# Optimization experiments

Hardware: AMD Instinct MI355X
Metric: run time of the kernel (lower is better)

Reference implementation:

```python
import jax, jax.numpy as jnp
import numpy as np

N = 50000   # function nodes
E = 100000  # edges per relation
H = 8       # heads
D = 96      # per-head dim (768 // 8)
L = 2       # conv layers
B = 256     # graphs in batch
C = 31      # num_classes + 1


def setup_inputs() -> dict:
    key = jax.random.key(0)
    ks = jax.random.split(key, 24)
    s = 0.05  # weight init scale to keep attention logits sane
    inp = {
        "function_feats": jax.random.normal(ks[0], (N, 768), jnp.float32),
        "w_src_calls": jax.random.normal(ks[1], (L, 768, 768), jnp.float32) * s,
        "b_src_calls": jnp.zeros((L, 768), jnp.float32),
        "w_dst_calls": jax.random.normal(ks[2], (L, 768, 768), jnp.float32) * s,
        "b_dst_calls": jnp.zeros((L, 768), jnp.float32),
        "attn_calls": jax.random.normal(ks[3], (L, H, D), jnp.float32) * s,
        "w_src_cb": jax.random.normal(ks[4], (L, 768, 768), jnp.float32) * s,
        "b_src_cb": jnp.zeros((L, 768), jnp.float32),
        "w_dst_cb": jax.random.normal(ks[5], (L, 768, 768), jnp.float32) * s,
        "b_dst_cb": jnp.zeros((L, 768), jnp.float32),
        "attn_cb": jax.random.normal(ks[6], (L, H, D), jnp.float32) * s,
        "fc1_w": jax.random.normal(ks[7], (768, 256), jnp.float32) * s,
        "fc1_b": jnp.zeros((256,), jnp.float32),
        "fc2_w": jax.random.normal(ks[8], (256, C), jnp.float32) * s,
        "fc2_b": jnp.zeros((C,), jnp.float32),
        "calls_src": jax.random.randint(ks[9], (E,), 0, N),
        "calls_dst": jax.random.randint(ks[10], (E,), 0, N),
        "cb_src": jax.random.randint(ks[11], (E,), 0, N),
        "cb_dst": jax.random.randint(ks[12], (E,), 0, N),
        "graph_start_idx": jnp.sort(jax.random.randint(ks[13], (B,), 0, N)),
        "labels": jax.random.randint(ks[14], (B,), 0, C),
    }
    return inp


def _gatv2(h, Ws, bs, Wd, bd, attn, src, dst):
    # DGL GATv2Conv: e_ij = attn . leaky_relu(W_src h_i + W_dst h_j); softmax over in-edges of j
    fs = (h @ Ws + bs).reshape(N, H, D)
    fd = (h @ Wd + bd).reshape(N, H, D)
    e = jax.nn.leaky_relu(fs[src] + fd[dst], negative_slope=0.2)  # [E,H,D]
    score = jnp.einsum('ehd,hd->eh', e, attn)                      # [E,H]
    mx = jax.ops.segment_max(score, dst, num_segments=N)           # [N,H]
    ex = jnp.exp(score - mx[dst])
    den = jax.ops.segment_sum(ex, dst, num_segments=N)
    alpha = ex / den[dst]                                          # edge softmax
    return jax.ops.segment_sum(fs[src] * alpha[..., None], dst, num_segments=N)  # [N,H,D]


def reference(function_feats, w_src_calls, b_src_calls, w_dst_calls, b_dst_calls,
              attn_calls, w_src_cb, b_src_cb, w_dst_cb, b_dst_cb, attn_cb,
              fc1_w, fc1_b, fc2_w, fc2_b,
              calls_src, calls_dst, cb_src, cb_dst, graph_start_idx, labels):
    h = function_feats
    for l in range(L):
        o = _gatv2(h, w_src_calls[l], b_src_calls[l], w_dst_calls[l], b_dst_calls[l],
                   attn_calls[l], calls_src, calls_dst)
        o = o + _gatv2(h, w_src_cb[l], b_src_cb[l], w_dst_cb[l], b_dst_cb[l],
                       attn_cb[l], cb_src, cb_dst)  # HeteroGraphConv 'sum' aggregate
        h = o.reshape(N, H * D) + h                  # residual
    func_embed = h[graph_start_idx]                  # [B,768] gather first node per graph
    logits = jax.nn.relu(func_embed @ fc1_w + fc1_b) @ fc2_w + fc2_b  # [B,C]
    logp = jax.nn.log_softmax(logits, axis=-1)
    loss = -jnp.mean(jnp.take_along_axis(logp, labels[:, None], axis=1))
    return (loss, logits)
```

## Files before the change

kernel.cpp:

```cpp
#include <hip/hip_runtime.h>
#include <hip/hip_bf16.h>
#include <math.h>

#define N_NODES 50000
#define NE      100000
#define FDIM    768
#define NFUSE   3072
#define NB      256
#define NC      31

#define A1_CAP  16384
#define N1_CAP  4096
#define NBLK    ((N_NODES + 255) / 256)
#define EB      ((NE + 255) / 256)
#define GTN     12

#define TWT_BLOCKS  (8 * 576)
#define BIAS_BLOCKS 24
#define CVT_BLOCKS  512
#define SETUP_BLOCKS (TWT_BLOCKS + BIAS_BLOCKS + CVT_BLOCKS)

typedef __hip_bfloat16 bf16;
typedef __attribute__((ext_vector_type(8))) short bf16x8;
typedef __attribute__((ext_vector_type(4))) float f32x4;

__device__ inline float u2f(unsigned short u) { return __uint_as_float(((unsigned int)u) << 16); }
__device__ inline unsigned short f2u(float f) { return __bfloat16_as_ushort(__float2bfloat16(f)); }

__device__ inline void load_lds16(const void* g, void* l) {
    __builtin_amdgcn_global_load_lds(
        (const __attribute__((address_space(1))) void*)g,
        (__attribute__((address_space(3))) void*)l, 16, 0, 0);
}

__global__ __launch_bounds__(256) void mark_gsi_kernel(const int* __restrict__ gsi,
                                                       int* __restrict__ fL2,
                                                       int* __restrict__ fL1,
                                                       int* __restrict__ fA1) {
    const int n = gsi[threadIdx.x];
    fL2[n] = 1; fL1[n] = 1; fA1[n] = 1;
}

__global__ __launch_bounds__(256) void mark2_kernel(const int* __restrict__ src0,
                                                    const int* __restrict__ dst0,
                                                    const int* __restrict__ src1,
                                                    const int* __restrict__ dst1,
                                                    const int* __restrict__ dflag,
                                                    int* __restrict__ f1,
                                                    int* __restrict__ f2) {
    const int e = blockIdx.x * 256 + threadIdx.x;
    if (e >= NE) return;
    const int* src = blockIdx.y ? src1 : src0;
    const int* dst = blockIdx.y ? dst1 : dst0;
    if (dflag[dst[e]]) {
        const int s = src[e];
        f1[s] = 1;
        if (f2) f2[s] = 1;
    }
}

__global__ __launch_bounds__(256) void comphist_kernel(const int* __restrict__ fA1,
                                                       const int* __restrict__ fL1,
                                                       const int* __restrict__ fL2,
                                                       int* __restrict__ list1, int* __restrict__ idx1,
                                                       int* __restrict__ list2, int* __restrict__ idx2,
                                                       int* __restrict__ list0,
                                                       int* __restrict__ cnts,
                                                       const int* __restrict__ dst0,
                                                       const int* __restrict__ dst1,
                                                       int* __restrict__ deg) {
    const int b = blockIdx.x, t = threadIdx.x;
    if (b < NBLK) {
        const int n = b * 256 + t;
        if (n >= N_NODES) return;
        if (fA1[n]) {
            const int p = atomicAdd(&cnts[0], 1);
            if (p < A1_CAP) { list1[p] = n; idx1[n] = p; } else idx1[n] = 0;
        }
        if (fL1[n]) {
            const int p = atomicAdd(&cnts[1], 1);
            if (p < N1_CAP) { list2[p] = n; idx2[n] = p; } else idx2[n] = 0;
        }
        if (fL2[n]) {
            const int p = atomicAdd(&cnts[2], 1);
            if (p < 256) list0[p] = n;
        }
    } else {
        const int eb_id = b - NBLK;
        const int r = (eb_id >= EB) ? 1 : 0;
        const int e = (eb_id - r * EB) * 256 + t;
        if (e < NE) atomicAdd(&deg[(size_t)r * N_NODES + (r ? dst1 : dst0)[e]], 1);
    }
}

__global__ __launch_bounds__(256) void setup_kernel(const float* __restrict__ w_sc,
                                                    const float* __restrict__ w_dc,
                                                    const float* __restrict__ w_scb,
                                                    const float* __restrict__ w_dcb,
                                                    const float* __restrict__ b_sc,
                                                    const float* __restrict__ b_dc,
                                                    const float* __restrict__ b_scb,
                                                    const float* __restrict__ b_dcb,
                                                    const float* __restrict__ feats,
                                                    const int* __restrict__ list,
                                                    const int* __restrict__ pcnt,
                                                    bf16* __restrict__ WtFl,
                                                    float* __restrict__ pb,
                                                    bf16* __restrict__ h) {
    __shared__ float tile[32][33];
    const int b = blockIdx.x;
    const int t = threadIdx.x;
    if (b < TWT_BLOCKS) {
        const int z = b / 576, cell = b % 576;
        const int l = z >> 2, sel2 = z & 3;
        const float* src;
        if (sel2 == 0) src = w_sc; else if (sel2 == 1) src = w_scb;
        else if (sel2 == 2) src = w_dc; else src = w_dcb;
        src += (size_t)l * FDIM * FDIM;
        bf16* dst = WtFl + (size_t)z * FDIM * FDIM;
        const int tx = t & 31, ty = t >> 5;
        const int x0 = (cell % 24) * 32, y0 = (cell / 24) * 32;
#pragma unroll
        for (int q = 0; q < 4; ++q)
            tile[ty + q * 8][tx] = src[(size_t)(y0 + ty + q * 8) * FDIM + x0 + tx];
        __syncthreads();
#pragma unroll
        for (int q = 0; q < 4; ++q)
            dst[(size_t)(x0 + ty + q * 8) * FDIM + y0 + tx] = __float2bfloat16(tile[tx][ty + q * 8]);
    } else if (b < TWT_BLOCKS + BIAS_BLOCKS) {
        const int idx = (b - TWT_BLOCKS) * 256 + t;
        const int l = idx / NFUSE, c = idx % NFUSE;
        const int sel2 = c / FDIM, off = c % FDIM;
        const float* src;
        if (sel2 == 0) src = b_sc; else if (sel2 == 1) src = b_scb;
        else if (sel2 == 2) src = b_dc; else src = b_dcb;
        pb[idx] = src[l * FDIM + off];
    } else {
        int c = *pcnt; if (c > A1_CAP) c = A1_CAP;
        for (int i = b - TWT_BLOCKS - BIAS_BLOCKS; i < c; i += CVT_BLOCKS) {
            const int n = list[i];
            const float* s = feats + (size_t)n * FDIM;
            bf16* d = h + (size_t)n * FDIM;
            for (int k = t; k < FDIM; k += 256) d[k] = __float2bfloat16(s[k]);
        }
    }
}

__global__ __launch_bounds__(256) void gemm2(const bf16* __restrict__ A,
                                             const bf16* __restrict__ Wt,
                                             const float* __restrict__ pb,
                                             bf16* __restrict__ C,
                                             const int* __restrict__ rlA,
                                             const int* __restrict__ cntAp, int capA,
                                             const int* __restrict__ rlB,
                                             const int* __restrict__ cntBp, int capB,
                                             const int* __restrict__ idxmap,
                                             int blocksA) {
    int bid = blockIdx.x;
    const int* rowlist;
    int cnt, col0;
    if (bid < blocksA) {
        rowlist = rlA; cnt = *cntAp; if (cnt > capA) cnt = capA; col0 = 0;
    } else {
        bid -= blocksA;
        rowlist = rlB; cnt = *cntBp; if (cnt > capB) cnt = capB; col0 = 1536;
    }
    const int tm = bid / GTN, tn = bid % GTN;
    const int m0 = tm * 128, n0 = tn * 128;
    if (m0 >= cnt) return;

    __shared__ __align__(16) short Abuf[128 * 64];
    __shared__ __align__(16) short Bbuf[128 * 64];
    const int t = threadIdx.x;
    const int wid = t >> 6, lane = t & 63;
    const int wr = wid >> 1, wc = wid & 1;
    const int lr = lane & 15, lk = lane >> 4;

    const f32x4 zero4 = {0.f, 0.f, 0.f, 0.f};
    f32x4 acc[4][4];
#pragma unroll
    for (int i = 0; i < 4; ++i)
#pragma unroll
        for (int j = 0; j < 4; ++j) acc[i][j] = zero4;

    int arow[4], brow[4], acol[4], ldsoff[4];
#pragma unroll
    for (int i = 0; i < 4; ++i) {
        const int s = i * 256 + t;
        const int rr = s >> 3, pch = s & 7;
        int ri = m0 + rr; if (ri >= cnt) ri = cnt - 1;
        arow[i] = rowlist[ri];
        brow[i] = col0 + n0 + rr;
        acol[i] = (pch ^ (rr & 7)) << 3;
        ldsoff[i] = (i * 256 + wid * 64) * 16;
    }

    for (int kt = 0; kt < FDIM / 64; ++kt) {
        const int k0 = kt * 64;
#pragma unroll
        for (int i = 0; i < 4; ++i) {
            load_lds16(A + (size_t)arow[i] * FDIM + k0 + acol[i], (char*)Abuf + ldsoff[i]);
            load_lds16(Wt + (size_t)brow[i] * FDIM + k0 + acol[i], (char*)Bbuf + ldsoff[i]);
        }
        __syncthreads();
#pragma unroll
        for (int kh = 0; kh < 2; ++kh) {
            bf16x8 av[4], bv[4];
            const int c = kh * 4 + lk;
#pragma unroll
            for (int i = 0; i < 4; ++i) {
                const int mm = wr * 64 + i * 16 + lr;
                av[i] = *(const bf16x8*)((const char*)Abuf + mm * 128 + ((c ^ (mm & 7)) << 4));
            }
#pragma unroll
            for (int j = 0; j < 4; ++j) {
                const int nn = wc * 64 + j * 16 + lr;
                bv[j] = *(const bf16x8*)((const char*)Bbuf + nn * 128 + ((c ^ (nn & 7)) << 4));
            }
#pragma unroll
            for (int i = 0; i < 4; ++i)
#pragma unroll
                for (int j = 0; j < 4; ++j)
                    acc[i][j] = __builtin_amdgcn_mfma_f32_16x16x32_bf16(bv[j], av[i], acc[i][j], 0, 0, 0);
        }
        __syncthreads();
    }

#pragma unroll
    for (int i = 0; i < 4; ++i) {
        const int row = m0 + wr * 64 + i * 16 + lr;
        if (row < cnt) {
            const int crow = idxmap[rowlist[row]];
#pragma unroll
            for (int j = 0; j < 4; ++j) {
                const int col = col0 + n0 + wc * 64 + j * 16 + lk * 4;
                const float4 b4 = *(const float4*)(pb + col);
                ushort4 w;
                w.x = f2u(acc[i][j][0] + b4.x);
                w.y = f2u(acc[i][j][1] + b4.y);
                w.z = f2u(acc[i][j][2] + b4.z);
                w.w = f2u(acc[i][j][3] + b4.w);
                *(ushort4*)(C + (size_t)crow * NFUSE + col) = w;
            }
        }
    }
}

__global__ __launch_bounds__(256) void scan1_kernel(const int* __restrict__ deg,
                                                    int* __restrict__ bsum) {
    const int r = blockIdx.y, b = blockIdx.x, t = threadIdx.x;
    const int i = b * 256 + t;
    __shared__ int s[256];
    s[t] = (i < N_NODES) ? deg[(size_t)r * N_NODES + i] : 0;
    __syncthreads();
    for (int o = 128; o > 0; o >>= 1) {
        if (t < o) s[t] += s[t + o];
        __syncthreads();
    }
    if (t == 0) bsum[r * NBLK + b] = s[0];
}

__global__ __launch_bounds__(256) void scan2_kernel(int* __restrict__ bsum,
                                                    int* __restrict__ boff,
                                                    int* __restrict__ rowp0,
                                                    int* __restrict__ rowp1) {
    const int t = threadIdx.x;
    if (t < 2) {
        int run = 0;
        for (int b = 0; b < NBLK; ++b) {
            boff[t * NBLK + b] = run;
            run += bsum[t * NBLK + b];
        }
    }
    if (t == 0) rowp0[N_NODES] = NE;
    if (t == 1) rowp1[N_NODES] = NE;
}

__global__ __launch_bounds__(256) void scan3_kernel(const int* __restrict__ deg,
                                                    const int* __restrict__ boff,
                                                    int* __restrict__ rowp0, int* __restrict__ cursor0,
                                                    int* __restrict__ rowp1, int* __restrict__ cursor1) {
    const int r = blockIdx.y, b = blockIdx.x, t = threadIdx.x;
    const int i = b * 256 + t;
    int* rowp = r ? rowp1 : rowp0;
    int* cursor = r ? cursor1 : cursor0;
    __shared__ int s[256];
    const int v = (i < N_NODES) ? deg[(size_t)r * N_NODES + i] : 0;
    s[t] = v;
    __syncthreads();
    for (int o = 1; o < 256; o <<= 1) {
        int x = 0;
        if (t >= o) x = s[t - o];
        __syncthreads();
        if (t >= o) s[t] += x;
        __syncthreads();
    }
    if (i < N_NODES) {
        const int p = boff[r * NBLK + b] + s[t] - v;
        rowp[i] = p;
        cursor[i] = p;
    }
}

__global__ __launch_bounds__(256) void scatter2_kernel(const int* __restrict__ dst0,
                                                       const int* __restrict__ dst1,
                                                       int* __restrict__ cursor0,
                                                       int* __restrict__ cursor1,
                                                       int* __restrict__ eid0,
                                                       int* __restrict__ eid1) {
    const int e = blockIdx.x * 256 + threadIdx.x;
    const int r = blockIdx.y;
    if (e < NE) {
        if (r == 0) { const int p = atomicAdd(&cursor0[dst0[e]], 1); eid0[p] = e; }
        else        { const int p = atomicAdd(&cursor1[dst1[e]], 1); eid1[p] = e; }
    }
}

__device__ inline void att_accum(const bf16* __restrict__ fsd, const int* __restrict__ idx,
                                 int n, int lane, const float* __restrict__ attn,
                                 const int* __restrict__ rowp, const int* __restrict__ eid,
                                 const int* __restrict__ src, int fs_off, int fd_off,
                                 float* __restrict__ out) {
    float fdv[12], atv[12];
    {
        const ushort4* pfd = (const ushort4*)(fsd + (size_t)idx[n] * NFUSE + fd_off + lane * 12);
        const ushort4 d0 = pfd[0], d1 = pfd[1], d2 = pfd[2];
        fdv[0] = u2f(d0.x); fdv[1] = u2f(d0.y); fdv[2] = u2f(d0.z); fdv[3] = u2f(d0.w);
        fdv[4] = u2f(d1.x); fdv[5] = u2f(d1.y); fdv[6] = u2f(d1.z); fdv[7] = u2f(d1.w);
        fdv[8] = u2f(d2.x); fdv[9] = u2f(d2.y); fdv[10] = u2f(d2.z); fdv[11] = u2f(d2.w);
        const float4* pat = (const float4*)(attn + lane * 12);
        const float4 a0 = pat[0], a1 = pat[1], a2 = pat[2];
        atv[0] = a0.x; atv[1] = a0.y; atv[2] = a0.z; atv[3] = a0.w;
        atv[4] = a1.x; atv[5] = a1.y; atv[6] = a1.z; atv[7] = a1.w;
        atv[8] = a2.x; atv[9] = a2.y; atv[10] = a2.z; atv[11] = a2.w;
    }
    const int beg = rowp[n], end = rowp[n + 1];
    float m = -INFINITY, den = 0.f;
    float acc[12];
#pragma unroll
    for (int j = 0; j < 12; ++j) acc[j] = 0.f;

    for (int i = beg; i < end; ++i) {
        const int e = eid[i];
        const ushort4* pf = (const ushort4*)(fsd + (size_t)idx[src[e]] * NFUSE + fs_off + lane * 12);
        const ushort4 a0 = pf[0], a1 = pf[1], a2 = pf[2];
        float fsv[12];
        fsv[0] = u2f(a0.x); fsv[1] = u2f(a0.y); fsv[2] = u2f(a0.z); fsv[3] = u2f(a0.w);
        fsv[4] = u2f(a1.x); fsv[5] = u2f(a1.y); fsv[6] = u2f(a1.z); fsv[7] = u2f(a1.w);
        fsv[8] = u2f(a2.x); fsv[9] = u2f(a2.y); fsv[10] = u2f(a2.z); fsv[11] = u2f(a2.w);
        float p = 0.f;
#pragma unroll
        for (int j = 0; j < 12; ++j) {
            float x = fsv[j] + fdv[j];
            x = (x > 0.f) ? x : 0.2f * x;
            p += x * atv[j];
        }
        p += __shfl_xor(p, 1);
        p += __shfl_xor(p, 2);
        p += __shfl_xor(p, 4);
        if (p > m) {
            const float sc = expf(m - p);
            den *= sc;
#pragma unroll
            for (int j = 0; j < 12; ++j) acc[j] *= sc;
            m = p;
        }
        const float w = expf(p - m);
        den += w;
#pragma unroll
        for (int j = 0; j < 12; ++j) acc[j] += w * fsv[j];
    }
    const float inv = (den > 0.f) ? 1.f / den : 0.f;
#pragma unroll
    for (int j = 0; j < 12; ++j) out[j] = acc[j] * inv;
}

__global__ __launch_bounds__(256) void aggL_kernel(const bf16* __restrict__ fsd,
                                                   const int* __restrict__ idx,
                                                   const float* __restrict__ attn0,
                                                   const float* __restrict__ attn1,
                                                   const int* __restrict__ rowp0,
                                                   const int* __restrict__ eid0,
                                                   const int* __restrict__ src0,
                                                   const int* __restrict__ rowp1,
                                                   const int* __restrict__ eid1,
                                                   const int* __restrict__ src1,
                                                   bf16* __restrict__ h,
                                                   const int* __restrict__ list,
                                                   const int* __restrict__ pcnt,
                                                   int cap) {
    const int wid = threadIdx.x >> 6;
    const int lane = threadIdx.x & 63;
    int cnt = *pcnt; if (cnt > cap) cnt = cap;
    const int i = blockIdx.x * 4 + wid;
    if (i >= cnt) return;
    const int n = list[i];

    float a0[12], a1[12];
    att_accum(fsd, idx, n, lane, attn0, rowp0, eid0, src0, 0, 1536, a0);
    att_accum(fsd, idx, n, lane, attn1, rowp1, eid1, src1, 768, 2304, a1);

    const size_t base = (size_t)n * FDIM + lane * 12;
    const ushort4* ph = (const ushort4*)(h + base);
    const ushort4 h0 = ph[0], h1 = ph[1], h2 = ph[2];
    ushort4 r0, r1, r2;
    r0.x = f2u(u2f(h0.x) + a0[0] + a1[0]);  r0.y = f2u(u2f(h0.y) + a0[1] + a1[1]);
    r0.z = f2u(u2f(h0.z) + a0[2] + a1[2]);  r0.w = f2u(u2f(h0.w) + a0[3] + a1[3]);
    r1.x = f2u(u2f(h1.x) + a0[4] + a1[4]);  r1.y = f2u(u2f(h1.y) + a0[5] + a1[5]);
    r1.z = f2u(u2f(h1.z) + a0[6] + a1[6]);  r1.w = f2u(u2f(h1.w) + a0[7] + a1[7]);
    r2.x = f2u(u2f(h2.x) + a0[8] + a1[8]);  r2.y = f2u(u2f(h2.y) + a0[9] + a1[9]);
    r2.z = f2u(u2f(h2.z) + a0[10] + a1[10]); r2.w = f2u(u2f(h2.w) + a0[11] + a1[11]);
    ((ushort4*)(h + base))[0] = r0; ((ushort4*)(h + base))[1] = r1; ((ushort4*)(h + base))[2] = r2;
}

__global__ __launch_bounds__(256) void head_kernel(const bf16* __restrict__ h,
                                                   const int* __restrict__ gsi,
                                                   const float* __restrict__ fc1w,
                                                   const float* __restrict__ fc1b,
                                                   const float* __restrict__ fc2w,
                                                   const float* __restrict__ fc2b,
                                                   float* __restrict__ out) {
    __shared__ float fe[FDIM];
    __shared__ float hid[256];
    const int b = blockIdx.x, t = threadIdx.x;
    const int node = gsi[b];
    for (int i = t; i < FDIM; i += 256) fe[i] = __bfloat162float(h[(size_t)node * FDIM + i]);
    __syncthreads();
    float acc = fc1b[t];
    for (int k = 0; k < FDIM; ++k) acc += fe[k] * fc1w[k * 256 + t];
    hid[t] = (acc > 0.f) ? acc : 0.f;
    __syncthreads();
    if (t < NC) {
        float acc2 = fc2b[t];
        for (int k = 0; k < 256; ++k) acc2 += hid[k] * fc2w[k * NC + t];
        out[1 + b * NC + t] = acc2;
    }
}

__global__ __launch_bounds__(256) void loss_kernel(const float* __restrict__ logits,
                                                   const int* __restrict__ labels,
                                                   float* __restrict__ out) {
    __shared__ float red[256];
    const int b = threadIdx.x;
    float m = -INFINITY;
    for (int c = 0; c < NC; ++c) m = fmaxf(m, logits[b * NC + c]);
    float sum = 0.f;
    for (int c = 0; c < NC; ++c) sum += expf(logits[b * NC + c] - m);
    const float lse = m + logf(sum);
    const float ll = logits[b * NC + labels[b]];
    red[b] = lse - ll;
    __syncthreads();
    for (int s = 128; s > 0; s >>= 1) {
        if (b < s) red[b] += red[b + s];
        __syncthreads();
    }
    if (b == 0) out[0] = red[0] / (float)NB;
}

extern "C" void kernel_launch(void* const* d_in, const int* in_sizes, int n_in,
                              void* d_out, int out_size, void* d_ws, size_t ws_size,
                              hipStream_t stream) {
    const float* feats = (const float*)d_in[0];
    const float* fc1w  = (const float*)d_in[11];
    const float* fc1b  = (const float*)d_in[12];
    const float* fc2w  = (const float*)d_in[13];
    const float* fc2b  = (const float*)d_in[14];
    const int* src0    = (const int*)d_in[15];
    const int* dst0    = (const int*)d_in[16];
    const int* src1    = (const int*)d_in[17];
    const int* dst1    = (const int*)d_in[18];
    const int* gsi     = (const int*)d_in[19];
    const int* labels  = (const int*)d_in[20];

    const size_t NF = (size_t)N_NODES * FDIM;
    const size_t WSZ = (size_t)FDIM * FDIM;
    char* p = (char*)d_ws;
    bf16* h    = (bf16*)p;  p += NF * 2;
    bf16* fsd  = (bf16*)p;  p += (size_t)A1_CAP * NFUSE * 2;
    bf16* WtFl = (bf16*)p;  p += 8 * WSZ * 2;
    float* pb  = (float*)p; p += 2 * NFUSE * 4;
    int* flagL2 = (int*)p;  p += (size_t)N_NODES * 4;
    int* flagL1 = (int*)p;  p += (size_t)N_NODES * 4;
    int* flagA1 = (int*)p;  p += (size_t)N_NODES * 4;
    int* cnts   = (int*)p;  p += 64 * 4;
    int* deg    = (int*)p;  p += 2 * (size_t)N_NODES * 4;
    const size_t zero_bytes = (3 * (size_t)N_NODES + 64 + 2 * (size_t)N_NODES) * 4;
    int* idx1  = (int*)p;   p += (size_t)N_NODES * 4;
    int* idx2  = (int*)p;   p += (size_t)N_NODES * 4;
    int* list1 = (int*)p;   p += (size_t)A1_CAP * 4;
    int* list2 = (int*)p;   p += (size_t)N1_CAP * 4;
    int* list0 = (int*)p;   p += 256 * 4;
    int* bsum  = (int*)p;   p += 2 * NBLK * 4;
    int* boff  = (int*)p;   p += 2 * NBLK * 4;
    int* rowp0 = (int*)p;   p += ((size_t)N_NODES + 1) * 4 + 252;
    int* rowp1 = (int*)p;   p += ((size_t)N_NODES + 1) * 4 + 252;
    int* cursor0 = (int*)p; p += (size_t)N_NODES * 4;
    int* cursor1 = (int*)p; p += (size_t)N_NODES * 4;
    int* eid0  = (int*)p;   p += (size_t)NE * 4;
    int* eid1  = (int*)p;   p += (size_t)NE * 4;

    hipMemsetAsync(flagL2, 0, zero_bytes, stream);
    mark_gsi_kernel<<<1, 256, 0, stream>>>(gsi, flagL2, flagL1, flagA1);
    mark2_kernel<<<dim3(EB, 2), 256, 0, stream>>>(src0, dst0, src1, dst1, flagL2, flagL1, flagA1);
    mark2_kernel<<<dim3(EB, 2), 256, 0, stream>>>(src0, dst0, src1, dst1, flagL1, flagA1, (int*)nullptr);
    comphist_kernel<<<NBLK + 2 * EB, 256, 0, stream>>>(
        flagA1, flagL1, flagL2, list1, idx1, list2, idx2, list0, cnts, dst0, dst1, deg);

    scan1_kernel<<<dim3(NBLK, 2), 256, 0, stream>>>(deg, bsum);
    scan2_kernel<<<1, 256, 0, stream>>>(bsum, boff, rowp0, rowp1);
    scan3_kernel<<<dim3(NBLK, 2), 256, 0, stream>>>(deg, boff, rowp0, cursor0, rowp1, cursor1);
    scatter2_kernel<<<dim3(EB, 2), 256, 0, stream>>>(dst0, dst1, cursor0, cursor1, eid0, eid1);

    setup_kernel<<<SETUP_BLOCKS, 256, 0, stream>>>(
        (const float*)d_in[1], (const float*)d_in[3], (const float*)d_in[6], (const float*)d_in[8],
        (const float*)d_in[2], (const float*)d_in[4], (const float*)d_in[7], (const float*)d_in[9],
        feats, list1, &cnts[0], WtFl, pb, h);

    const int blocksA0 = (A1_CAP / 128) * GTN;
    const int blocksB0 = (N1_CAP / 128) * GTN;
    const int blocksA1 = (N1_CAP / 128) * GTN;
    const int blocksB1 = (256 / 128) * GTN;

    gemm2<<<blocksA0 + blocksB0, 256, 0, stream>>>(
        h, WtFl, pb, fsd,
        list1, &cnts[0], A1_CAP, list2, &cnts[1], N1_CAP, idx1, blocksA0);
    aggL_kernel<<<(N1_CAP + 3) / 4, 256, 0, stream>>>(
        fsd, idx1, (const float*)d_in[5], (const float*)d_in[10],
        rowp0, eid0, src0, rowp1, eid1, src1, h, list2, &cnts[1], N1_CAP);

    gemm2<<<blocksA1 + blocksB1, 256, 0, stream>>>(
        h, WtFl + 4 * WSZ, pb + NFUSE, fsd,
        list2, &cnts[1], N1_CAP, list0, &cnts[2], 256, idx2, blocksA1);
    aggL_kernel<<<64, 256, 0, stream>>>(
        fsd, idx2, (const float*)d_in[5] + FDIM, (const float*)d_in[10] + FDIM,
        rowp0, eid0, src0, rowp1, eid1, src1, h, list0, &cnts[2], 256);

    head_kernel<<<NB, 256, 0, stream>>>(h, gsi, fc1w, fc1b, fc2w, fc2b, (float*)d_out);
    loss_kernel<<<1, 256, 0, stream>>>((float*)d_out + 1, labels, (float*)d_out);
}
```

Baseline: 192.4 us.

## Build CSR only for needed destination nodes and fuse final aggregation into head

```diff
diff --git a/kernel.cpp b/kernel.cpp
--- a/kernel.cpp
+++ b/kernel.cpp
@@ -19,6 +19,7 @@
 #define BIAS_BLOCKS 24
 #define CVT_BLOCKS  512
 #define SETUP_BLOCKS (TWT_BLOCKS + BIAS_BLOCKS + CVT_BLOCKS)
+#define SETUPH_BLOCKS (SETUP_BLOCKS + 2 * EB)
 
 typedef __hip_bfloat16 bf16;
 typedef __attribute__((ext_vector_type(8))) short bf16x8;
@@ -33,63 +34,68 @@
         (__attribute__((address_space(3))) void*)l, 16, 0, 0);
 }
 
-__global__ __launch_bounds__(256) void mark_gsi_kernel(const int* __restrict__ gsi,
-                                                       int* __restrict__ fL2,
-                                                       int* __restrict__ fL1,
-                                                       int* __restrict__ fA1) {
-    const int n = gsi[threadIdx.x];
-    fL2[n] = 1; fL1[n] = 1; fA1[n] = 1;
-}
-
-__global__ __launch_bounds__(256) void mark2_kernel(const int* __restrict__ src0,
+__global__ __launch_bounds__(256) void markA_kernel(const int* __restrict__ gsi,
+                                                    const int* __restrict__ src0,
                                                     const int* __restrict__ dst0,
                                                     const int* __restrict__ src1,
                                                     const int* __restrict__ dst1,
-                                                    const int* __restrict__ dflag,
-                                                    int* __restrict__ f1,
-                                                    int* __restrict__ f2) {
+                                                    int* __restrict__ fL1,
+                                                    int* __restrict__ fA1,
+                                                    int* __restrict__ list0,
+                                                    int* __restrict__ cnts) {
+    const int t = threadIdx.x, b = blockIdx.x;
+    if (b == 0) {
+        const int n = gsi[t];
+        fL1[n] = 1; fA1[n] = 1;
+        const bool first = (t == 0) || (gsi[t - 1] != n);
+        if (first) {
+            const int p = atomicAdd(&cnts[2], 1);
+            if (p < 256) list0[p] = n;
+        }
+        return;
+    }
+    __shared__ int g[256];
+    g[t] = gsi[t];
+    __syncthreads();
+    const int eb = b - 1;
+    const int r = (eb >= EB) ? 1 : 0;
+    const int e = (eb - r * EB) * 256 + t;
+    if (e >= NE) return;
+    const int d = (r ? dst1 : dst0)[e];
+    int lo = 0, hi = 256;
+    while (lo < hi) { const int mid = (lo + hi) >> 1; if (g[mid] < d) lo = mid + 1; else hi = mid; }
+    if (lo < 256 && g[lo] == d) {
+        const int s = (r ? src1 : src0)[e];
+        fL1[s] = 1; fA1[s] = 1;
+    }
+}
+
+__global__ __launch_bounds__(256) void markB_kernel(const int* __restrict__ src0,
+                                                    const int* __restrict__ dst0,
+                                                    const int* __restrict__ src1,
+                                                    const int* __restrict__ dst1,
+                                                    const int* __restrict__ fL1,
+                                                    int* __restrict__ fA1) {
     const int e = blockIdx.x * 256 + threadIdx.x;
     if (e >= NE) return;
-    const int* src = blockIdx.y ? src1 : src0;
-    const int* dst = blockIdx.y ? dst1 : dst0;
-    if (dflag[dst[e]]) {
-        const int s = src[e];
-        f1[s] = 1;
-        if (f2) f2[s] = 1;
-    }
-}
-
-__global__ __launch_bounds__(256) void comphist_kernel(const int* __restrict__ fA1,
-                                                       const int* __restrict__ fL1,
-                                                       const int* __restrict__ fL2,
-                                                       int* __restrict__ list1, int* __restrict__ idx1,
-                                                       int* __restrict__ list2, int* __restrict__ idx2,
-                                                       int* __restrict__ list0,
-                                                       int* __restrict__ cnts,
-                                                       const int* __restrict__ dst0,
-                                                       const int* __restrict__ dst1,
-                                                       int* __restrict__ deg) {
-    const int b = blockIdx.x, t = threadIdx.x;
-    if (b < NBLK) {
-        const int n = b * 256 + t;
-        if (n >= N_NODES) return;
-        if (fA1[n]) {
-            const int p = atomicAdd(&cnts[0], 1);
-            if (p < A1_CAP) { list1[p] = n; idx1[n] = p; } else idx1[n] = 0;
-        }
-        if (fL1[n]) {
-            const int p = atomicAdd(&cnts[1], 1);
-            if (p < N1_CAP) { list2[p] = n; idx2[n] = p; } else idx2[n] = 0;
-        }
-        if (fL2[n]) {
-            const int p = atomicAdd(&cnts[2], 1);
-            if (p < 256) list0[p] = n;
-        }
-    } else {
-        const int eb_id = b - NBLK;
-        const int r = (eb_id >= EB) ? 1 : 0;
-        const int e = (eb_id - r * EB) * 256 + t;
-        if (e < NE) atomicAdd(&deg[(size_t)r * N_NODES + (r ? dst1 : dst0)[e]], 1);
+    const int r = blockIdx.y;
+    if (fL1[(r ? dst1 : dst0)[e]]) fA1[(r ? src1 : src0)[e]] = 1;
+}
+
+__global__ __launch_bounds__(256) void compact_kernel(const int* __restrict__ fA1,
+                                                      const int* __restrict__ fL1,
+                                                      int* __restrict__ list1, int* __restrict__ idx1,
+                                                      int* __restrict__ list2, int* __restrict__ idx2,
+                                                      int* __restrict__ cnts) {
+    const int n = blockIdx.x * 256 + threadIdx.x;
+    if (n >= N_NODES) return;
+    if (fA1[n]) {
+        const int p = atomicAdd(&cnts[0], 1);
+        if (p < A1_CAP) { list1[p] = n; idx1[n] = p; } else idx1[n] = 0;
+    }
+    if (fL1[n]) {
+        const int p = atomicAdd(&cnts[1], 1);
+        if (p < N1_CAP) { list2[p] = n; idx2[n] = p; } else idx2[n] = 0;
     }
 }
 
@@ -106,7 +112,12 @@
                                                     const int* __restrict__ pcnt,
                                                     bf16* __restrict__ WtFl,
                                                     float* __restrict__ pb,
-                                                    bf16* __restrict__ h) {
+                                                    bf16* __restrict__ h,
+                                                    const int* __restrict__ dst0,
+                                                    const int* __restrict__ dst1,
+                                                    const int* __restrict__ fL1,
+                                                    const int* __restrict__ idx2,
+                                                    int* __restrict__ dega) {
     __shared__ float tile[32][33];
     const int b = blockIdx.x;
     const int t = threadIdx.x;
@@ -135,7 +146,7 @@
         if (sel2 == 0) src = b_sc; else if (sel2 == 1) src = b_scb;
         else if (sel2 == 2) src = b_dc; else src = b_dcb;
         pb[idx] = src[l * FDIM + off];
-    } else {
+    } else if (b < SETUP_BLOCKS) {
         int c = *pcnt; if (c > A1_CAP) c = A1_CAP;
         for (int i = b - TWT_BLOCKS - BIAS_BLOCKS; i < c; i += CVT_BLOCKS) {
             const int n = list[i];
@@ -143,6 +154,62 @@
             bf16* d = h + (size_t)n * FDIM;
             for (int k = t; k < FDIM; k += 256) d[k] = __float2bfloat16(s[k]);
         }
+    } else {
+        const int eb = b - SETUP_BLOCKS;
+        const int r = (eb >= EB) ? 1 : 0;
+        const int e = (eb - r * EB) * 256 + t;
+        if (e < NE) {
+            const int d = (r ? dst1 : dst0)[e];
+            if (fL1[d]) atomicAdd(&dega[r * N1_CAP + idx2[d]], 1);
+        }
+    }
+}
+
+__global__ __launch_bounds__(256) void scana_kernel(const int* __restrict__ dega,
+                                                    int* __restrict__ rowpa,
+                                                    int* __restrict__ cursora) {
+    __shared__ int part[256];
+    const int t = threadIdx.x;
+    for (int r = 0; r < 2; ++r) {
+        const int base = r * N1_CAP;
+        int loc[16];
+        int s = 0;
+#pragma unroll
+        for (int q = 0; q < 16; ++q) { loc[q] = dega[base + t * 16 + q]; s += loc[q]; }
+        part[t] = s;
+        __syncthreads();
+        for (int o = 1; o < 256; o <<= 1) {
+            int x = (t >= o) ? part[t - o] : 0;
+            __syncthreads();
+            part[t] += x;
+            __syncthreads();
+        }
+        int run = part[t] - s;
+        const int rbase = r * (N1_CAP + 1);
+#pragma unroll
+        for (int q = 0; q < 16; ++q) {
+            rowpa[rbase + t * 16 + q] = run;
+            cursora[base + t * 16 + q] = run;
+            run += loc[q];
+        }
+        if (t == 255) rowpa[rbase + N1_CAP] = run;
+        __syncthreads();
+    }
+}
+
+__global__ __launch_bounds__(256) void scattera_kernel(const int* __restrict__ dst0,
+                                                       const int* __restrict__ dst1,
+                                                       const int* __restrict__ fL1,
+                                                       const int* __restrict__ idx2,
+                                                       int* __restrict__ cursora,
+                                                       int* __restrict__ eida) {
+    const int e = blockIdx.x * 256 + threadIdx.x;
+    if (e >= NE) return;
+    const int r = blockIdx.y;
+    const int d = (r ? dst1 : dst0)[e];
+    if (fL1[d]) {
+        const int p = atomicAdd(&cursora[r * N1_CAP + idx2[d]], 1);
+        eida[(size_t)r * NE + p] = e;
     }
 }
 
@@ -246,84 +313,14 @@
     }
 }
 
-__global__ __launch_bounds__(256) void scan1_kernel(const int* __restrict__ deg,
-                                                    int* __restrict__ bsum) {
-    const int r = blockIdx.y, b = blockIdx.x, t = threadIdx.x;
-    const int i = b * 256 + t;
-    __shared__ int s[256];
-    s[t] = (i < N_NODES) ? deg[(size_t)r * N_NODES + i] : 0;
-    __syncthreads();
-    for (int o = 128; o > 0; o >>= 1) {
-        if (t < o) s[t] += s[t + o];
-        __syncthreads();
-    }
-    if (t == 0) bsum[r * NBLK + b] = s[0];
-}
-
-__global__ __launch_bounds__(256) void scan2_kernel(int* __restrict__ bsum,
-                                                    int* __restrict__ boff,
-                                                    int* __restrict__ rowp0,
-                                                    int* __restrict__ rowp1) {
-    const int t = threadIdx.x;
-    if (t < 2) {
-        int run = 0;
-        for (int b = 0; b < NBLK; ++b) {
-            boff[t * NBLK + b] = run;
-            run += bsum[t * NBLK + b];
-        }
-    }
-    if (t == 0) rowp0[N_NODES] = NE;
-    if (t == 1) rowp1[N_NODES] = NE;
-}
-
-__global__ __launch_bounds__(256) void scan3_kernel(const int* __restrict__ deg,
-                                                    const int* __restrict__ boff,
-                                                    int* __restrict__ rowp0, int* __restrict__ cursor0,
-                                                    int* __restrict__ rowp1, int* __restrict__ cursor1) {
-    const int r = blockIdx.y, b = blockIdx.x, t = threadIdx.x;
-    const int i = b * 256 + t;
-    int* rowp = r ? rowp1 : rowp0;
-    int* cursor = r ? cursor1 : cursor0;
-    __shared__ int s[256];
-    const int v = (i < N_NODES) ? deg[(size_t)r * N_NODES + i] : 0;
-    s[t] = v;
-    __syncthreads();
-    for (int o = 1; o < 256; o <<= 1) {
-        int x = 0;
-        if (t >= o) x = s[t - o];
-        __syncthreads();
-        if (t >= o) s[t] += x;
-        __syncthreads();
-    }
-    if (i < N_NODES) {
-        const int p = boff[r * NBLK + b] + s[t] - v;
-        rowp[i] = p;
-        cursor[i] = p;
-    }
-}
-
-__global__ __launch_bounds__(256) void scatter2_kernel(const int* __restrict__ dst0,
-                                                       const int* __restrict__ dst1,
-                                                       int* __restrict__ cursor0,
-                                                       int* __restrict__ cursor1,
-                                                       int* __restrict__ eid0,
-                                                       int* __restrict__ eid1) {
-    const int e = blockIdx.x * 256 + threadIdx.x;
-    const int r = blockIdx.y;
-    if (e < NE) {
-        if (r == 0) { const int p = atomicAdd(&cursor0[dst0[e]], 1); eid0[p] = e; }
-        else        { const int p = atomicAdd(&cursor1[dst1[e]], 1); eid1[p] = e; }
-    }
-}
-
-__device__ inline void att_accum(const bf16* __restrict__ fsd, const int* __restrict__ idx,
-                                 int n, int lane, const float* __restrict__ attn,
-                                 const int* __restrict__ rowp, const int* __restrict__ eid,
-                                 const int* __restrict__ src, int fs_off, int fd_off,
-                                 float* __restrict__ out) {
+__device__ inline void att_accum(const bf16* __restrict__ fsd, const int* __restrict__ idxsrc,
+                                 int fdrow, int lane, const float* __restrict__ attn,
+                                 int beg, int end,
+                                 const int* __restrict__ eid, const int* __restrict__ src,
+                                 int fs_off, int fd_off, float* __restrict__ out) {
     float fdv[12], atv[12];
     {
-        const ushort4* pfd = (const ushort4*)(fsd + (size_t)idx[n] * NFUSE + fd_off + lane * 12);
+        const ushort4* pfd = (const ushort4*)(fsd + (size_t)fdrow * NFUSE + fd_off + lane * 12);
         const ushort4 d0 = pfd[0], d1 = pfd[1], d2 = pfd[2];
         fdv[0] = u2f(d0.x); fdv[1] = u2f(d0.y); fdv[2] = u2f(d0.z); fdv[3] = u2f(d0.w);
         fdv[4] = u2f(d1.x); fdv[5] = u2f(d1.y); fdv[6] = u2f(d1.z); fdv[7] = u2f(d1.w);
@@ -334,7 +331,6 @@
         atv[4] = a1.x; atv[5] = a1.y; atv[6] = a1.z; atv[7] = a1.w;
         atv[8] = a2.x; atv[9] = a2.y; atv[10] = a2.z; atv[11] = a2.w;
     }
-    const int beg = rowp[n], end = rowp[n + 1];
     float m = -INFINITY, den = 0.f;
     float acc[12];
 #pragma unroll
@@ -342,7 +338,7 @@
 
     for (int i = beg; i < end; ++i) {
         const int e = eid[i];
-        const ushort4* pf = (const ushort4*)(fsd + (size_t)idx[src[e]] * NFUSE + fs_off + lane * 12);
+        const ushort4* pf = (const ushort4*)(fsd + (size_t)idxsrc[src[e]] * NFUSE + fs_off + lane * 12);
         const ushort4 a0 = pf[0], a1 = pf[1], a2 = pf[2];
         float fsv[12];
         fsv[0] = u2f(a0.x); fsv[1] = u2f(a0.y); fsv[2] = u2f(a0.z); fsv[3] = u2f(a0.w);
@@ -376,29 +372,29 @@
 }
 
 __global__ __launch_bounds__(256) void aggL_kernel(const bf16* __restrict__ fsd,
-                                                   const int* __restrict__ idx,
+                                                   const int* __restrict__ idx1,
                                                    const float* __restrict__ attn0,
                                                    const float* __restrict__ attn1,
-                                                   const int* __restrict__ rowp0,
-                                                   const int* __restrict__ eid0,
+                                                   const int* __restrict__ rowpa,
+                                                   const int* __restrict__ eida,
                                                    const int* __restrict__ src0,
-                                                   const int* __restrict__ rowp1,
-                                                   const int* __restrict__ eid1,
                                                    const int* __restrict__ src1,
                                                    bf16* __restrict__ h,
-                                                   const int* __restrict__ list,
-                                                   const int* __restrict__ pcnt,
-                                                   int cap) {
+                                                   const int* __restrict__ list2,
+                                                   const int* __restrict__ pcnt) {
     const int wid = threadIdx.x >> 6;
     const int lane = threadIdx.x & 63;
-    int cnt = *pcnt; if (cnt > cap) cnt = cap;
+    int cnt = *pcnt; if (cnt > N1_CAP) cnt = N1_CAP;
     const int i = blockIdx.x * 4 + wid;
     if (i >= cnt) return;
-    const int n = list[i];
+    const int n = list2[i];
+    const int fdrow = idx1[n];
 
     float a0[12], a1[12];
-    att_accum(fsd, idx, n, lane, attn0, rowp0, eid0, src0, 0, 1536, a0);
-    att_accum(fsd, idx, n, lane, attn1, rowp1, eid1, src1, 768, 2304, a1);
+    att_accum(fsd, idx1, fdrow, lane, attn0, rowpa[i], rowpa[i + 1],
+              eida, src0, 0, 1536, a0);
+    att_accum(fsd, idx1, fdrow, lane, attn1, rowpa[(N1_CAP + 1) + i], rowpa[(N1_CAP + 1) + i + 1],
+              eida + NE, src1, 768, 2304, a1);
 
     const size_t base = (size_t)n * FDIM + lane * 12;
     const ushort4* ph = (const ushort4*)(h + base);
@@ -413,27 +409,50 @@
     ((ushort4*)(h + base))[0] = r0; ((ushort4*)(h + base))[1] = r1; ((ushort4*)(h + base))[2] = r2;
 }
 
-__global__ __launch_bounds__(256) void head_kernel(const bf16* __restrict__ h,
-                                                   const int* __restrict__ gsi,
-                                                   const float* __restrict__ fc1w,
-                                                   const float* __restrict__ fc1b,
-                                                   const float* __restrict__ fc2w,
-                                                   const float* __restrict__ fc2b,
-                                                   float* __restrict__ out) {
-    __shared__ float fe[FDIM];
+__global__ __launch_bounds__(256) void agghead_kernel(const bf16* __restrict__ fsd,
+                                                      const int* __restrict__ idx2,
+                                                      const float* __restrict__ attn0,
+                                                      const float* __restrict__ attn1,
+                                                      const int* __restrict__ rowpa,
+                                                      const int* __restrict__ eida,
+                                                      const int* __restrict__ src0,
+                                                      const int* __restrict__ src1,
+                                                      const bf16* __restrict__ h,
+                                                      const int* __restrict__ gsi,
+                                                      const float* __restrict__ fc1w,
+                                                      const float* __restrict__ fc1b,
+                                                      const float* __restrict__ fc2w,
+                                                      const float* __restrict__ fc2b,
+                                                      float* __restrict__ out) {
+    __shared__ float a0s[FDIM], a1s[FDIM], fe[FDIM];
     __shared__ float hid[256];
     const int b = blockIdx.x, t = threadIdx.x;
-    const int node = gsi[b];
-    for (int i = t; i < FDIM; i += 256) fe[i] = __bfloat162float(h[(size_t)node * FDIM + i]);
+    const int n = gsi[b];
+    const int wv = t >> 6, lane = t & 63;
+    if (wv < 2) {
+        const int j = idx2[n];
+        const int rb = wv * (N1_CAP + 1);
+        float a[12];
+        att_accum(fsd, idx2, j, lane, wv ? attn1 : attn0,
+                  rowpa[rb + j], rowpa[rb + j + 1],
+                  eida + (size_t)wv * NE, wv ? src1 : src0,
+                  wv ? 768 : 0, wv ? 2304 : 1536, a);
+        float* dl = wv ? a1s : a0s;
+#pragma unroll
+        for (int q = 0; q < 12; ++q) dl[lane * 12 + q] = a[q];
+    }
+    __syncthreads();
+    for (int d = t; d < FDIM; d += 256)
+        fe[d] = u2f(__bfloat16_as_ushort(h[(size_t)n * FDIM + d])) + a0s[d] + a1s[d];
     __syncthreads();
     float acc = fc1b[t];
     for (int k = 0; k < FDIM; ++k) acc += fe[k] * fc1w[k * 256 + t];
     hid[t] = (acc > 0.f) ? acc : 0.f;
     __syncthreads();
     if (t < NC) {
-        float acc2 = fc2b[t];
-        for (int k = 0; k < 256; ++k) acc2 += hid[k] * fc2w[k * NC + t];
-        out[1 + b * NC + t] = acc2;
+        float a2 = fc2b[t];
+        for (int k = 0; k < 256; ++k) a2 += hid[k] * fc2w[k * NC + t];
+        out[1 + b * NC + t] = a2;
     }
 }
 
@@ -479,42 +498,30 @@
     bf16* fsd  = (bf16*)p;  p += (size_t)A1_CAP * NFUSE * 2;
     bf16* WtFl = (bf16*)p;  p += 8 * WSZ * 2;
     float* pb  = (float*)p; p += 2 * NFUSE * 4;
-    int* flagL2 = (int*)p;  p += (size_t)N_NODES * 4;
-    int* flagL1 = (int*)p;  p += (size_t)N_NODES * 4;
-    int* flagA1 = (int*)p;  p += (size_t)N_NODES * 4;
-    int* cnts   = (int*)p;  p += 64 * 4;
-    int* deg    = (int*)p;  p += 2 * (size_t)N_NODES * 4;
-    const size_t zero_bytes = (3 * (size_t)N_NODES + 64 + 2 * (size_t)N_NODES) * 4;
+    int* fA1  = (int*)p;    p += (size_t)N_NODES * 4;
+    int* fL1  = (int*)p;    p += (size_t)N_NODES * 4;
+    int* cnts = (int*)p;    p += 64 * 4;
+    int* dega = (int*)p;    p += 2 * (size_t)N1_CAP * 4;
+    const size_t zero_bytes = (2 * (size_t)N_NODES + 64 + 2 * (size_t)N1_CAP) * 4;
     int* idx1  = (int*)p;   p += (size_t)N_NODES * 4;
     int* idx2  = (int*)p;   p += (size_t)N_NODES * 4;
     int* list1 = (int*)p;   p += (size_t)A1_CAP * 4;
     int* list2 = (int*)p;   p += (size_t)N1_CAP * 4;
     int* list0 = (int*)p;   p += 256 * 4;
-    int* bsum  = (int*)p;   p += 2 * NBLK * 4;
-    int* boff  = (int*)p;   p += 2 * NBLK * 4;
-    int* rowp0 = (int*)p;   p += ((size_t)N_NODES + 1) * 4 + 252;
-    int* rowp1 = (int*)p;   p += ((size_t)N_NODES + 1) * 4 + 252;
-    int* cursor0 = (int*)p; p += (size_t)N_NODES * 4;
-    int* cursor1 = (int*)p; p += (size_t)N_NODES * 4;
-    int* eid0  = (int*)p;   p += (size_t)NE * 4;
-    int* eid1  = (int*)p;   p += (size_t)NE * 4;
-
-    hipMemsetAsync(flagL2, 0, zero_bytes, stream);
-    mark_gsi_kernel<<<1, 256, 0, stream>>>(gsi, flagL2, flagL1, flagA1);
-    mark2_kernel<<<dim3(EB, 2), 256, 0, stream>>>(src0, dst0, src1, dst1, flagL2, flagL1, flagA1);
-    mark2_kernel<<<dim3(EB, 2), 256, 0, stream>>>(src0, dst0, src1, dst1, flagL1, flagA1, (int*)nullptr);
-    comphist_kernel<<<NBLK + 2 * EB, 256, 0, stream>>>(
-        flagA1, flagL1, flagL2, list1, idx1, list2, idx2, list0, cnts, dst0, dst1, deg);
-
-    scan1_kernel<<<dim3(NBLK, 2), 256, 0, stream>>>(deg, bsum);
-    scan2_kernel<<<1, 256, 0, stream>>>(bsum, boff, rowp0, rowp1);
-    scan3_kernel<<<dim3(NBLK, 2), 256, 0, stream>>>(deg, boff, rowp0, cursor0, rowp1, cursor1);
-    scatter2_kernel<<<dim3(EB, 2), 256, 0, stream>>>(dst0, dst1, cursor0, cursor1, eid0, eid1);
-
-    setup_kernel<<<SETUP_BLOCKS, 256, 0, stream>>>(
+    int* rowpa = (int*)p;   p += 2 * ((size_t)N1_CAP + 1) * 4;
+    int* cursora = (int*)p; p += 2 * (size_t)N1_CAP * 4;
+    int* eida  = (int*)p;   p += 2 * (size_t)NE * 4;
+
+    hipMemsetAsync(fA1, 0, zero_bytes, stream);
+    markA_kernel<<<1 + 2 * EB, 256, 0, stream>>>(gsi, src0, dst0, src1, dst1, fL1, fA1, list0, cnts);
+    markB_kernel<<<dim3(EB, 2), 256, 0, stream>>>(src0, dst0, src1, dst1, fL1, fA1);
+    compact_kernel<<<NBLK, 256, 0, stream>>>(fA1, fL1, list1, idx1, list2, idx2, cnts);
+    setup_kernel<<<SETUPH_BLOCKS, 256, 0, stream>>>(
         (const float*)d_in[1], (const float*)d_in[3], (const float*)d_in[6], (const float*)d_in[8],
         (const float*)d_in[2], (const float*)d_in[4], (const float*)d_in[7], (const float*)d_in[9],
-        feats, list1, &cnts[0], WtFl, pb, h);
+        feats, list1, &cnts[0], WtFl, pb, h, dst0, dst1, fL1, idx2, dega);
+    scana_kernel<<<1, 256, 0, stream>>>(dega, rowpa, cursora);
+    scattera_kernel<<<dim3(EB, 2), 256, 0, stream>>>(dst0, dst1, fL1, idx2, cursora, eida);
 
     const int blocksA0 = (A1_CAP / 128) * GTN;
     const int blocksB0 = (N1_CAP / 128) * GTN;
@@ -526,15 +533,14 @@
         list1, &cnts[0], A1_CAP, list2, &cnts[1], N1_CAP, idx1, blocksA0);
     aggL_kernel<<<(N1_CAP + 3) / 4, 256, 0, stream>>>(
         fsd, idx1, (const float*)d_in[5], (const float*)d_in[10],
-        rowp0, eid0, src0, rowp1, eid1, src1, h, list2, &cnts[1], N1_CAP);
+        rowpa, eida, src0, src1, h, list2, &cnts[1]);
 
     gemm2<<<blocksA1 + blocksB1, 256, 0, stream>>>(
         h, WtFl + 4 * WSZ, pb + NFUSE, fsd,
         list2, &cnts[1], N1_CAP, list0, &cnts[2], 256, idx2, blocksA1);
-    aggL_kernel<<<64, 256, 0, stream>>>(
+    agghead_kernel<<<NB, 256, 0, stream>>>(
         fsd, idx2, (const float*)d_in[5] + FDIM, (const float*)d_in[10] + FDIM,
-        rowp0, eid0, src0, rowp1, eid1, src1, h, list0, &cnts[2], 256);
-
-    head_kernel<<<NB, 256, 0, stream>>>(h, gsi, fc1w, fc1b, fc2w, fc2b, (float*)d_out);
+        rowpa, eida, src0, src1, h, gsi, fc1w, fc1b, fc2w, fc2b, (float*)d_out);
+
     loss_kernel<<<1, 256, 0, stream>>>((float*)d_out + 1, labels, (float*)d_out);
 }
```

After: 159.5 us. -17.1%, faster.
